# Kernel tuning notes

Hardware: AMD Instinct MI355X
Metric: run time of the kernel (lower is better)

## Reference

```python
import jax, jax.numpy as jnp
import numpy as np

WIN = 8          # window side -> N = 64 tokens per window
HEADS = 8
NCAV = 2
EGO_DIST_BINS = 4
EGO_ANGLE_BINS = 4


def _rel_pos_index(wh, ww):
    # Swin-style relative position index, (wh*ww, wh*ww) int
    coords = np.stack(np.meshgrid(np.arange(wh), np.arange(ww), indexing='ij'))  # (2,wh,ww)
    flat = coords.reshape(2, -1)
    rel = (flat[:, :, None] - flat[:, None, :]).transpose(1, 2, 0).astype(np.int64)
    rel[:, :, 0] += wh - 1
    rel[:, :, 1] += ww - 1
    rel[:, :, 0] *= 2 * ww - 1
    return jnp.asarray(rel.sum(-1))


def _ego_bias_index(affine_matrix, H, W):
    # per-(cav,window) bin index into ego_position_bias_table
    gy, gx = jnp.meshgrid(jnp.arange(H // WIN), jnp.arange(W // WIN), indexing='ij')
    centers = jnp.stack([gx * WIN + WIN / 2.0, gy * WIN + WIN / 2.0], axis=-1)
    centers = centers.reshape(-1, 2).astype(jnp.float32)              # (nW, 2)
    img_c = jnp.array([[W / 2.0], [H / 2.0]], jnp.float32)            # (2, 1)
    ego = (affine_matrix[:, :2, :2] @ img_c + affine_matrix[:, :2, 2:3])[..., 0]  # (ncav, 2)
    rel = centers[None, :, :] - ego[:, None, :]                        # (ncav, nW, 2)
    dist = jnp.linalg.norm(rel, axis=-1)
    ang = jnp.arctan2(rel[..., 1], rel[..., 0])
    db = (dist / (dist.max() + 1e-6) * (EGO_DIST_BINS - 1)).astype(jnp.int32)
    ab = ((ang + jnp.pi) / (2 * jnp.pi) * (EGO_ANGLE_BINS - 1)).astype(jnp.int32)
    return (db * EGO_ANGLE_BINS + ab).reshape(-1)                      # (ncav*nW,) == (B_,)


def setup_inputs() -> dict:
    key = jax.random.key(0)
    ks = jax.random.split(key, 10)
    H = W = 256
    B_ = NCAV * (H // WIN) * (W // WIN)   # 2048
    N = WIN * WIN                          # 64
    C = 256
    s = 0.02
    return {
        'x': jax.random.normal(ks[0], (B_, N, C), jnp.float32),
        'affine_matrix': jax.random.normal(ks[1], (NCAV, 2, 3), jnp.float32),
        'Wq': jax.random.normal(ks[2], (C, C), jnp.float32) * s,
        'bq': jax.random.normal(ks[3], (C,), jnp.float32) * s,
        'Wkv': jax.random.normal(ks[4], (C, 2 * C), jnp.float32) * s,
        'bkv': jax.random.normal(ks[5], (2 * C,), jnp.float32) * s,
        'Wp': jax.random.normal(ks[6], (C, C), jnp.float32) * s,
        'bp': jax.random.normal(ks[7], (C,), jnp.float32) * s,
        'rel_table': jax.random.normal(ks[8], ((2 * WIN - 1) ** 2, HEADS), jnp.float32) * s,
        'ego_table': jax.random.normal(ks[9], (EGO_DIST_BINS * EGO_ANGLE_BINS, HEADS), jnp.float32) * s,
        'w': jnp.ones((2,), jnp.float32),
        'H': H,
        'W': W,
    }


def reference(x, affine_matrix, Wq, bq, Wkv, bkv, Wp, bp, rel_table, ego_table, w, H, W):
    B_, N, C = x.shape
    h = HEADS
    hd = C // h
    scale = hd ** -0.5

    q = (x @ Wq + bq).reshape(B_, N, h, hd).transpose(0, 2, 1, 3)          # (B_, h, N, hd)
    kv = (x @ Wkv + bkv).reshape(B_, N, 2, h, hd).transpose(2, 0, 3, 1, 4)
    k, v = kv[0], kv[1]                                                     # (B_, h, N, hd)

    attn = jnp.einsum('bhnd,bhmd->bhnm', q * scale, k)                      # (B_, h, N, N)

    # Swin relative position bias
    rpi = _rel_pos_index(WIN, WIN)
    rel_bias = rel_table[rpi.reshape(-1)].reshape(N, N, h).transpose(2, 0, 1)  # (h, N, N)

    # ego-relative bias: one scalar per (window, head), broadcast over NxN
    idx = _ego_bias_index(affine_matrix, H, W)                              # (B_,)
    ego_bias = ego_table[idx]                                               # (B_, h)

    attn = attn + rel_bias[None, :, :, :] + ego_bias[:, :, None, None]

    attn0 = jax.nn.softmax(attn, axis=-1)
    attn1 = jnp.square(jnp.maximum(attn, 0.0))   # relu(attn)**2 (no-mask branch)
    ws = jax.nn.softmax(w)
    attn = attn0 * ws[0] + attn1 * ws[1]

    out = jnp.einsum('bhnm,bhmd->bhnd', attn, v).transpose(0, 2, 1, 3).reshape(B_, N, C)
    return out @ Wp + bp
```

## Files before the change

### kernel.cpp

```cpp
#include <hip/hip_runtime.h>

#define NT   64
#define CDIM 256
#define NHEAD 8
#define SCALE 0.17677669529663687f
#define PI_F 3.14159265358979f

typedef short bfrag __attribute__((ext_vector_type(8)));
typedef float f4    __attribute__((ext_vector_type(4)));
typedef unsigned short us4 __attribute__((ext_vector_type(4)));

__device__ __forceinline__ unsigned short f2bf(float f){
  unsigned u = __builtin_bit_cast(unsigned, f);
  u += 0x7FFFu + ((u >> 16) & 1u);
  return (unsigned short)(u >> 16);
}
__device__ __forceinline__ unsigned pk2(float a, float b){
  return (unsigned)f2bf(a) | ((unsigned)f2bf(b) << 16);
}
__device__ __forceinline__ f4 mfma16(bfrag a, bfrag b, f4 c){
  return __builtin_amdgcn_mfma_f32_16x16x32_bf16(a, b, c, 0, 0, 0);
}
__device__ __forceinline__ int swx(int row, int u){ return (row << 5) + (u ^ (row & 7)); }

__device__ __forceinline__ bfrag xpose(f4 m0, f4 m1, int quad, int cc){
  int P0m0 = (int)pk2(m0[0], m0[1]);
  int P1m0 = (int)pk2(m0[2], m0[3]);
  int P0m1 = (int)pk2(m1[0], m1[1]);
  int P1m1 = (int)pk2(m1[2], m1[3]);
  int srcA = ((quad & 1) << 5) + cc;
  int srcB = srcA + 16;
  int hi = quad >> 1;
  int a0 = __shfl(P0m0, srcA, 64), a1 = __shfl(P0m1, srcA, 64);
  int b0 = __shfl(P1m0, srcA, 64), b1 = __shfl(P1m1, srcA, 64);
  int c0 = __shfl(P0m0, srcB, 64), c1 = __shfl(P0m1, srcB, 64);
  int d0 = __shfl(P1m0, srcB, 64), d1 = __shfl(P1m1, srcB, 64);
  union { bfrag f; int u[4]; } r;
  r.u[0] = hi ? a1 : a0;
  r.u[1] = hi ? b1 : b0;
  r.u[2] = hi ? c1 : c0;
  r.u[3] = hi ? d1 : d0;
  return r.f;
}

__device__ __forceinline__ void subgemm32(const unsigned short* __restrict__ wt,
                                          const unsigned short* lx,
                                          const float* __restrict__ bqkv,
                                          int ocb, int tb, int quad, int cc,
                                          bfrag& f0, bfrag& f1)
{
  f4 acc[2][2];
  acc[0][0] = (f4){0,0,0,0}; acc[0][1] = (f4){0,0,0,0};
  acc[1][0] = (f4){0,0,0,0}; acc[1][1] = (f4){0,0,0,0};
  #pragma unroll
  for (int ks = 0; ks < 8; ++ks){
    bfrag a0 = *(const bfrag*)(wt + (ocb +      cc)*256 + ks*32 + quad*8);
    bfrag a1 = *(const bfrag*)(wt + (ocb + 16 + cc)*256 + ks*32 + quad*8);
    bfrag b0 = *(const bfrag*)(&lx[swx(tb +      cc, ks*4 + quad)*8]);
    bfrag b1 = *(const bfrag*)(&lx[swx(tb + 16 + cc, ks*4 + quad)*8]);
    acc[0][0] = mfma16(a0, b0, acc[0][0]);
    acc[0][1] = mfma16(a0, b1, acc[0][1]);
    acc[1][0] = mfma16(a1, b0, acc[1][0]);
    acc[1][1] = mfma16(a1, b1, acc[1][1]);
  }
  #pragma unroll
  for (int mt = 0; mt < 2; ++mt)
    #pragma unroll
    for (int r = 0; r < 4; ++r){
      float bb = bqkv[ocb + mt*16 + quad*4 + r];
      acc[mt][0][r] += bb;
      acc[mt][1][r] += bb;
    }
  f0 = xpose(acc[0][0], acc[1][0], quad, cc);
  f1 = xpose(acc[0][1], acc[1][1], quad, cc);
}

__device__ __forceinline__ void logits_it(bfrag aq, const bfrag* kf,
    int iibase, int quad, int cc, int h,
    const float* __restrict__ relt, float ego,
    f4 (&SA)[4], float (&Z)[4])
{
  #pragma unroll
  for (int jt = 0; jt < 4; ++jt){
    f4 z = (f4){0,0,0,0};
    SA[jt] = mfma16(aq, kf[jt], z);
  }
  #pragma unroll
  for (int jt = 0; jt < 4; ++jt){
    int jj = jt*16 + cc;
    int yj = jj >> 3, xj = jj & 7;
    #pragma unroll
    for (int r = 0; r < 4; ++r){
      int ii = iibase + r;
      int ridx = ((ii >> 3) - yj + 7)*15 + ((ii & 7) - xj + 7);
      SA[jt][r] += relt[ridx*8 + h] + ego;
    }
  }
  #pragma unroll
  for (int r = 0; r < 4; ++r){
    float m = fmaxf(fmaxf(SA[0][r], SA[1][r]), fmaxf(SA[2][r], SA[3][r]));
    for (int off = 1; off < 16; off <<= 1) m = fmaxf(m, __shfl_xor(m, off, 64));
    float s = 0.0f;
    #pragma unroll
    for (int jt = 0; jt < 4; ++jt) s += __expf(SA[jt][r] - m);
    for (int off = 1; off < 16; off <<= 1) s += __shfl_xor(s, off, 64);
    Z[r] = m + __logf(s);
  }
}

__device__ __forceinline__ void pv_it(const f4 (&SA)[4], const float (&Z)[4],
    int quad, int cc, unsigned short* Pt, const unsigned short* vts,
    float ws0, float ws1, f4* yit)
{
  #pragma unroll
  for (int chunk = 0; chunk < 2; ++chunk){
    #pragma unroll
    for (int jtl = 0; jtl < 2; ++jtl){
      int jt = chunk*2 + jtl;
      #pragma unroll
      for (int r = 0; r < 4; ++r){
        float av = SA[jt][r];
        float rl = fmaxf(av, 0.0f);
        float p = ws0 * __expf(av - Z[r]) + ws1 * rl * rl;
        Pt[(quad*4 + r)*32 + jtl*16 + cc] = f2bf(p);
      }
    }
    bfrag pa = *(const bfrag*)(&Pt[cc*32 + quad*8]);
    #pragma unroll
    for (int nt = 0; nt < 2; ++nt){
      int row = nt*16 + cc;
      bfrag pb = *(const bfrag*)(&vts[row*64 + (((chunk*4 + quad) ^ (row & 7)) << 3)]);
      yit[nt] = mfma16(pa, pb, yit[nt]);
    }
  }
}

__global__ void prep_kernel(const float* __restrict__ Wq,  const float* __restrict__ bq,
                            const float* __restrict__ Wkv, const float* __restrict__ bkv,
                            const float* __restrict__ Wp,
                            unsigned short* __restrict__ wt, float* __restrict__ bqkv)
{
  const int bid = blockIdx.x, tid = threadIdx.x;
  if (bid < 256) {
    __shared__ float t[32][33];
    const int r0 = (bid >> 3) * 32;
    const int c0 = (bid & 7) * 32;
    const int rl = tid & 31, ch = tid >> 5;
    for (int k = 0; k < 4; ++k){
      int c = c0 + ch + k*8, r = r0 + rl;
      float v;
      if (r < 256)      v = Wq[c*256 + r] * SCALE;
      else if (r < 768) v = Wkv[c*512 + (r - 256)];
      else              v = Wp[c*256 + (r - 768)];
      t[rl][ch + k*8] = v;
    }
    __syncthreads();
    for (int k = 0; k < 4; ++k){
      int orr = ch + k*8;
      wt[(r0 + orr)*256 + c0 + rl] = f2bf(t[orr][rl]);
    }
  } else {
    for (int j = tid; j < 768; j += 256)
      bqkv[j] = (j < 256) ? bq[j]*SCALE : bkv[j - 256];
  }
}

__global__ __launch_bounds__(512, 4) void attn_kernel(
    const float* __restrict__ x, const float* __restrict__ wvec,
    const float* __restrict__ bp, float* __restrict__ out,
    const unsigned short* __restrict__ wt, const float* __restrict__ bqkv,
    const float* __restrict__ relt, const float* __restrict__ egot,
    const float* __restrict__ aff)
{
  __shared__ unsigned short ldsX[NT*CDIM];
  __shared__ unsigned short ldsV[NHEAD*2048];
  __shared__ unsigned short ldsP[NHEAD*512];

  const int b = blockIdx.x;
  const int tid = threadIdx.x;
  const int wv = tid >> 6, lane = tid & 63;
  const int quad = lane >> 4, cc = lane & 15;
  const int h = wv;

  const float4* xg = (const float4*)(x + (size_t)b*(NT*CDIM));
  #pragma unroll
  for (int it = 0; it < 8; ++it){
    int i4 = tid + it*512;
    float4 v = xg[i4];
    us4 pk = { f2bf(v.x), f2bf(v.y), f2bf(v.z), f2bf(v.w) };
    int row = i4 >> 6, u = (i4 & 63) >> 1, hf = i4 & 1;
    *(us4*)(&ldsX[swx(row, u)*8 + hf*4]) = pk;
  }
  float w0 = wvec[0], w1 = wvec[1];
  float wm = fmaxf(w0, w1);
  float e0 = __expf(w0 - wm), e1 = __expf(w1 - wm);
  float ws0 = e0/(e0+e1), ws1 = e1/(e0+e1);
  float ego;
  {
    float ex0=(aff[0]+aff[1])*128.f+aff[2],  ey0=(aff[3]+aff[4])*128.f+aff[5];
    float ex1=(aff[6]+aff[7])*128.f+aff[8],  ey1=(aff[9]+aff[10])*128.f+aff[11];
    float dmax = 0.f;
    #pragma unroll
    for (int c = 0; c < 4; ++c){
      float cx = (c & 1) ? 252.f : 4.f, cy = (c >> 1) ? 252.f : 4.f;
      float d0x=cx-ex0, d0y=cy-ey0, d1x=cx-ex1, d1y=cy-ey1;
      dmax = fmaxf(dmax, fmaxf(sqrtf(d0x*d0x+d0y*d0y), sqrtf(d1x*d1x+d1y*d1y)));
    }
    dmax += 1e-6f;
    int cv = b >> 10, wi = b & 1023;
    float cx = (float)((wi & 31)*8 + 4), cy = (float)((wi >> 5)*8 + 4);
    float ex = cv ? ex1 : ex0, ey = cv ? ey1 : ey0;
    float dx = cx - ex, dy = cy - ey;
    float dd = sqrtf(dx*dx + dy*dy);
    float ang = atan2f(dy, dx);
    int db = (int)(dd/dmax*3.0f);
    int ab = (int)((ang + PI_F)/(2.0f*PI_F)*3.0f);
    ego = egot[(db*4 + ab)*8 + h];
  }
  __syncthreads();

  bfrag aq[4], kf[4];
  subgemm32(wt, ldsX, bqkv, h*32,       0,  quad, cc, aq[0], aq[1]);
  subgemm32(wt, ldsX, bqkv, h*32,       32, quad, cc, aq[2], aq[3]);
  subgemm32(wt, ldsX, bqkv, 256 + h*32, 0,  quad, cc, kf[0], kf[1]);
  subgemm32(wt, ldsX, bqkv, 256 + h*32, 32, quad, cc, kf[2], kf[3]);
  unsigned short* vs = &ldsV[wv*2048];
  {
    const int ocb = 512 + h*32;
    #pragma unroll
    for (int tb = 0; tb < 64; tb += 32){
      f4 vacc[2][2];
      vacc[0][0] = (f4){0,0,0,0}; vacc[0][1] = (f4){0,0,0,0};
      vacc[1][0] = (f4){0,0,0,0}; vacc[1][1] = (f4){0,0,0,0};
      #pragma unroll
      for (int ks = 0; ks < 8; ++ks){
        bfrag a0 = *(const bfrag*)(wt + (ocb +      cc)*256 + ks*32 + quad*8);
        bfrag a1 = *(const bfrag*)(wt + (ocb + 16 + cc)*256 + ks*32 + quad*8);
        bfrag b0 = *(const bfrag*)(&ldsX[swx(tb +      cc, ks*4 + quad)*8]);
        bfrag b1 = *(const bfrag*)(&ldsX[swx(tb + 16 + cc, ks*4 + quad)*8]);
        vacc[0][0] = mfma16(a0, b0, vacc[0][0]);
        vacc[0][1] = mfma16(a0, b1, vacc[0][1]);
        vacc[1][0] = mfma16(a1, b0, vacc[1][0]);
        vacc[1][1] = mfma16(a1, b1, vacc[1][1]);
      }
      #pragma unroll
      for (int mt = 0; mt < 2; ++mt)
        #pragma unroll
        for (int ntl = 0; ntl < 2; ++ntl){
          int tok = tb + ntl*16 + cc;
          int tu = tok >> 3, te = tok & 7;
          #pragma unroll
          for (int r = 0; r < 4; ++r){
            int d = mt*16 + quad*4 + r;
            vs[d*64 + ((tu ^ (d & 7)) << 3) + te] =
                f2bf(vacc[mt][ntl][r] + bqkv[ocb + d]);
          }
        }
    }
  }

  f4 yacc[4][2];
  #pragma unroll
  for (int it = 0; it < 4; ++it){
    yacc[it][0] = (f4){0,0,0,0}; yacc[it][1] = (f4){0,0,0,0};
  }
  unsigned short* Pt = &ldsP[wv*512];
  #pragma unroll
  for (int it = 0; it < 4; ++it){
    f4 SA[4]; float Z[4];
    logits_it(aq[it], kf, it*16 + quad*4, quad, cc, h, relt, ego, SA, Z);
    pv_it(SA, Z, quad, cc, Pt, vs, ws0, ws1, yacc[it]);
  }
  __syncthreads();

  #pragma unroll
  for (int it = 0; it < 4; ++it)
    #pragma unroll
    for (int nt = 0; nt < 2; ++nt)
      #pragma unroll
      for (int r = 0; r < 4; ++r){
        int ii = it*16 + quad*4 + r;
        int col = h*32 + nt*16 + cc;
        ldsX[swx(ii, col>>3)*8 + (col&7)] = f2bf(yacc[it][nt][r]);
      }
  __syncthreads();

  {
    const int mt = wv & 3;
    const int cb = (wv >> 2)*128;
    f4 o[8];
    #pragma unroll
    for (int nt = 0; nt < 8; ++nt) o[nt] = (f4){0,0,0,0};
    #pragma unroll
    for (int ks = 0; ks < 8; ++ks){
      bfrag ay = *(const bfrag*)(&ldsX[swx(mt*16 + cc, ks*4 + quad)*8]);
      #pragma unroll
      for (int nt = 0; nt < 8; ++nt){
        bfrag bw = *(const bfrag*)(wt + (768 + cb + nt*16 + cc)*256 + ks*32 + quad*8);
        o[nt] = mfma16(ay, bw, o[nt]);
      }
    }
    float* og = out + (size_t)b*(NT*CDIM);
    #pragma unroll
    for (int nt = 0; nt < 8; ++nt){
      int col = cb + nt*16 + cc;
      float bpv = bp[col];
      #pragma unroll
      for (int r = 0; r < 4; ++r){
        int tok = mt*16 + quad*4 + r;
        og[tok*256 + col] = o[nt][r] + bpv;
      }
    }
  }
}

extern "C" void kernel_launch(void* const* d_in, const int* in_sizes, int n_in,
                              void* d_out, int out_size, void* d_ws, size_t ws_size,
                              hipStream_t stream)
{
  const float* x    = (const float*)d_in[0];
  const float* aff  = (const float*)d_in[1];
  const float* Wq   = (const float*)d_in[2];
  const float* bq   = (const float*)d_in[3];
  const float* Wkv  = (const float*)d_in[4];
  const float* bkv  = (const float*)d_in[5];
  const float* Wp   = (const float*)d_in[6];
  const float* bp   = (const float*)d_in[7];
  const float* relt = (const float*)d_in[8];
  const float* egot = (const float*)d_in[9];
  const float* w    = (const float*)d_in[10];
  float* out = (float*)d_out;

  char* ws = (char*)d_ws;
  unsigned short* wt = (unsigned short*)ws;
  float* bqkv = (float*)(ws + 524288);

  hipLaunchKernelGGL(prep_kernel, dim3(257), dim3(256), 0, stream,
                     Wq, bq, Wkv, bkv, Wp, wt, bqkv);
  hipLaunchKernelGGL(attn_kernel, dim3(2048), dim3(512), 0, stream,
                     x, w, bp, out, wt, bqkv, relt, egot, aff);
}
```

Before: 570.5 us.

## Keep V and P in registers via transposed MFMA, drop LDS staging buffers

The V projection is computed in the transposed orientation and kept as register fragments via lane shuffles, so the per-head V and P staging buffers in shared memory are no longer needed. Logits are computed as K·Q^T so each lane holds a full query column, which turns the softmax reductions into two cross-quad shuffles. The probabilities are turned into MFMA operands with shuffles rather than an LDS round trip, and the attention output is written to LDS in MFMA-fragment order so the output projection reads it directly. This cuts LDS traffic and footprint, which may allow more blocks per CU, at the cost of more shuffles and register pressure.

```diff
diff --git a/kernel.cpp b/kernel.cpp
--- a/kernel.cpp
+++ b/kernel.cpp
@@ -49,90 +49,28 @@
                                           int ocb, int tb, int quad, int cc,
                                           bfrag& f0, bfrag& f1)
 {
-  f4 acc[2][2];
-  acc[0][0] = (f4){0,0,0,0}; acc[0][1] = (f4){0,0,0,0};
-  acc[1][0] = (f4){0,0,0,0}; acc[1][1] = (f4){0,0,0,0};
+  f4 acc00 = (f4){0,0,0,0}, acc01 = (f4){0,0,0,0};
+  f4 acc10 = (f4){0,0,0,0}, acc11 = (f4){0,0,0,0};
   #pragma unroll
   for (int ks = 0; ks < 8; ++ks){
     bfrag a0 = *(const bfrag*)(wt + (ocb +      cc)*256 + ks*32 + quad*8);
     bfrag a1 = *(const bfrag*)(wt + (ocb + 16 + cc)*256 + ks*32 + quad*8);
     bfrag b0 = *(const bfrag*)(&lx[swx(tb +      cc, ks*4 + quad)*8]);
     bfrag b1 = *(const bfrag*)(&lx[swx(tb + 16 + cc, ks*4 + quad)*8]);
-    acc[0][0] = mfma16(a0, b0, acc[0][0]);
-    acc[0][1] = mfma16(a0, b1, acc[0][1]);
-    acc[1][0] = mfma16(a1, b0, acc[1][0]);
-    acc[1][1] = mfma16(a1, b1, acc[1][1]);
-  }
-  #pragma unroll
-  for (int mt = 0; mt < 2; ++mt)
-    #pragma unroll
-    for (int r = 0; r < 4; ++r){
-      float bb = bqkv[ocb + mt*16 + quad*4 + r];
-      acc[mt][0][r] += bb;
-      acc[mt][1][r] += bb;
-    }
-  f0 = xpose(acc[0][0], acc[1][0], quad, cc);
-  f1 = xpose(acc[0][1], acc[1][1], quad, cc);
-}
-
-__device__ __forceinline__ void logits_it(bfrag aq, const bfrag* kf,
-    int iibase, int quad, int cc, int h,
-    const float* __restrict__ relt, float ego,
-    f4 (&SA)[4], float (&Z)[4])
-{
-  #pragma unroll
-  for (int jt = 0; jt < 4; ++jt){
-    f4 z = (f4){0,0,0,0};
-    SA[jt] = mfma16(aq, kf[jt], z);
-  }
-  #pragma unroll
-  for (int jt = 0; jt < 4; ++jt){
-    int jj = jt*16 + cc;
-    int yj = jj >> 3, xj = jj & 7;
-    #pragma unroll
-    for (int r = 0; r < 4; ++r){
-      int ii = iibase + r;
-      int ridx = ((ii >> 3) - yj + 7)*15 + ((ii & 7) - xj + 7);
-      SA[jt][r] += relt[ridx*8 + h] + ego;
-    }
+    acc00 = mfma16(a0, b0, acc00);
+    acc01 = mfma16(a0, b1, acc01);
+    acc10 = mfma16(a1, b0, acc10);
+    acc11 = mfma16(a1, b1, acc11);
   }
   #pragma unroll
   for (int r = 0; r < 4; ++r){
-    float m = fmaxf(fmaxf(SA[0][r], SA[1][r]), fmaxf(SA[2][r], SA[3][r]));
-    for (int off = 1; off < 16; off <<= 1) m = fmaxf(m, __shfl_xor(m, off, 64));
-    float s = 0.0f;
-    #pragma unroll
-    for (int jt = 0; jt < 4; ++jt) s += __expf(SA[jt][r] - m);
-    for (int off = 1; off < 16; off <<= 1) s += __shfl_xor(s, off, 64);
-    Z[r] = m + __logf(s);
-  }
-}
-
-__device__ __forceinline__ void pv_it(const f4 (&SA)[4], const float (&Z)[4],
-    int quad, int cc, unsigned short* Pt, const unsigned short* vts,
-    float ws0, float ws1, f4* yit)
-{
-  #pragma unroll
-  for (int chunk = 0; chunk < 2; ++chunk){
-    #pragma unroll
-    for (int jtl = 0; jtl < 2; ++jtl){
-      int jt = chunk*2 + jtl;
-      #pragma unroll
-      for (int r = 0; r < 4; ++r){
-        float av = SA[jt][r];
-        float rl = fmaxf(av, 0.0f);
-        float p = ws0 * __expf(av - Z[r]) + ws1 * rl * rl;
-        Pt[(quad*4 + r)*32 + jtl*16 + cc] = f2bf(p);
-      }
-    }
-    bfrag pa = *(const bfrag*)(&Pt[cc*32 + quad*8]);
-    #pragma unroll
-    for (int nt = 0; nt < 2; ++nt){
-      int row = nt*16 + cc;
-      bfrag pb = *(const bfrag*)(&vts[row*64 + (((chunk*4 + quad) ^ (row & 7)) << 3)]);
-      yit[nt] = mfma16(pa, pb, yit[nt]);
-    }
-  }
+    float bb0 = bqkv[ocb +      quad*4 + r];
+    float bb1 = bqkv[ocb + 16 + quad*4 + r];
+    acc00[r] += bb0; acc01[r] += bb0;
+    acc10[r] += bb1; acc11[r] += bb1;
+  }
+  f0 = xpose(acc00, acc10, quad, cc);
+  f1 = xpose(acc01, acc11, quad, cc);
 }
 
 __global__ void prep_kernel(const float* __restrict__ Wq,  const float* __restrict__ bq,
@@ -173,8 +111,6 @@
     const float* __restrict__ aff)
 {
   __shared__ unsigned short ldsX[NT*CDIM];
-  __shared__ unsigned short ldsV[NHEAD*2048];
-  __shared__ unsigned short ldsP[NHEAD*512];
 
   const int b = blockIdx.x;
   const int tid = threadIdx.x;
@@ -219,70 +155,85 @@
   }
   __syncthreads();
 
-  bfrag aq[4], kf[4];
-  subgemm32(wt, ldsX, bqkv, h*32,       0,  quad, cc, aq[0], aq[1]);
-  subgemm32(wt, ldsX, bqkv, h*32,       32, quad, cc, aq[2], aq[3]);
+  bfrag qf[4], kf[4], vf[4];
+  subgemm32(wt, ldsX, bqkv, h*32,       0,  quad, cc, qf[0], qf[1]);
+  subgemm32(wt, ldsX, bqkv, h*32,       32, quad, cc, qf[2], qf[3]);
   subgemm32(wt, ldsX, bqkv, 256 + h*32, 0,  quad, cc, kf[0], kf[1]);
   subgemm32(wt, ldsX, bqkv, 256 + h*32, 32, quad, cc, kf[2], kf[3]);
-  unsigned short* vs = &ldsV[wv*2048];
-  {
-    const int ocb = 512 + h*32;
-    #pragma unroll
-    for (int tb = 0; tb < 64; tb += 32){
-      f4 vacc[2][2];
-      vacc[0][0] = (f4){0,0,0,0}; vacc[0][1] = (f4){0,0,0,0};
-      vacc[1][0] = (f4){0,0,0,0}; vacc[1][1] = (f4){0,0,0,0};
-      #pragma unroll
-      for (int ks = 0; ks < 8; ++ks){
-        bfrag a0 = *(const bfrag*)(wt + (ocb +      cc)*256 + ks*32 + quad*8);
-        bfrag a1 = *(const bfrag*)(wt + (ocb + 16 + cc)*256 + ks*32 + quad*8);
-        bfrag b0 = *(const bfrag*)(&ldsX[swx(tb +      cc, ks*4 + quad)*8]);
-        bfrag b1 = *(const bfrag*)(&ldsX[swx(tb + 16 + cc, ks*4 + quad)*8]);
-        vacc[0][0] = mfma16(a0, b0, vacc[0][0]);
-        vacc[0][1] = mfma16(a0, b1, vacc[0][1]);
-        vacc[1][0] = mfma16(a1, b0, vacc[1][0]);
-        vacc[1][1] = mfma16(a1, b1, vacc[1][1]);
-      }
-      #pragma unroll
-      for (int mt = 0; mt < 2; ++mt)
-        #pragma unroll
-        for (int ntl = 0; ntl < 2; ++ntl){
-          int tok = tb + ntl*16 + cc;
-          int tu = tok >> 3, te = tok & 7;
-          #pragma unroll
-          for (int r = 0; r < 4; ++r){
-            int d = mt*16 + quad*4 + r;
-            vs[d*64 + ((tu ^ (d & 7)) << 3) + te] =
-                f2bf(vacc[mt][ntl][r] + bqkv[ocb + d]);
-          }
-        }
-    }
-  }
-
-  f4 yacc[4][2];
-  #pragma unroll
-  for (int it = 0; it < 4; ++it){
-    yacc[it][0] = (f4){0,0,0,0}; yacc[it][1] = (f4){0,0,0,0};
-  }
-  unsigned short* Pt = &ldsP[wv*512];
-  #pragma unroll
-  for (int it = 0; it < 4; ++it){
-    f4 SA[4]; float Z[4];
-    logits_it(aq[it], kf, it*16 + quad*4, quad, cc, h, relt, ego, SA, Z);
-    pv_it(SA, Z, quad, cc, Pt, vs, ws0, ws1, yacc[it]);
+  #pragma unroll
+  for (int chunk = 0; chunk < 2; ++chunk){
+    int tb = chunk*32;
+    f4 acc00 = (f4){0,0,0,0}, acc01 = (f4){0,0,0,0};
+    f4 acc10 = (f4){0,0,0,0}, acc11 = (f4){0,0,0,0};
+    #pragma unroll
+    for (int ks = 0; ks < 8; ++ks){
+      bfrag x0 = *(const bfrag*)(&ldsX[swx(tb +      cc, ks*4 + quad)*8]);
+      bfrag x1 = *(const bfrag*)(&ldsX[swx(tb + 16 + cc, ks*4 + quad)*8]);
+      bfrag w0f = *(const bfrag*)(wt + (512 + h*32 +      cc)*256 + ks*32 + quad*8);
+      bfrag w1f = *(const bfrag*)(wt + (512 + h*32 + 16 + cc)*256 + ks*32 + quad*8);
+      acc00 = mfma16(x0, w0f, acc00);
+      acc01 = mfma16(x0, w1f, acc01);
+      acc10 = mfma16(x1, w0f, acc10);
+      acc11 = mfma16(x1, w1f, acc11);
+    }
+    float bb0 = bqkv[512 + h*32 +      cc];
+    float bb1 = bqkv[512 + h*32 + 16 + cc];
+    #pragma unroll
+    for (int r = 0; r < 4; ++r){
+      acc00[r] += bb0; acc10[r] += bb0;
+      acc01[r] += bb1; acc11[r] += bb1;
+    }
+    vf[chunk*2 + 0] = xpose(acc00, acc10, quad, cc);
+    vf[chunk*2 + 1] = xpose(acc01, acc11, quad, cc);
   }
   __syncthreads();
 
-  #pragma unroll
-  for (int it = 0; it < 4; ++it)
-    #pragma unroll
-    for (int nt = 0; nt < 2; ++nt)
+  const f4 z4 = (f4){0,0,0,0};
+  #pragma unroll
+  for (int qt = 0; qt < 4; ++qt){
+    f4 SA[4];
+    #pragma unroll
+    for (int kt = 0; kt < 4; ++kt) SA[kt] = mfma16(kf[kt], qf[qt], z4);
+    int ii = qt*16 + cc;
+    int yi = ii >> 3, xi = ii & 7;
+    #pragma unroll
+    for (int kt = 0; kt < 4; ++kt)
       #pragma unroll
       for (int r = 0; r < 4; ++r){
-        int ii = it*16 + quad*4 + r;
-        int col = h*32 + nt*16 + cc;
-        ldsX[swx(ii, col>>3)*8 + (col&7)] = f2bf(yacc[it][nt][r]);
-      }
+        int jj = kt*16 + quad*4 + r;
+        int ridx = (yi - (jj >> 3) + 7)*15 + (xi - (jj & 7) + 7);
+        SA[kt][r] += relt[ridx*8 + h] + ego;
+      }
+    float m = -1e30f;
+    #pragma unroll
+    for (int kt = 0; kt < 4; ++kt)
+      #pragma unroll
+      for (int r = 0; r < 4; ++r) m = fmaxf(m, SA[kt][r]);
+    m = fmaxf(m, __shfl_xor(m, 16, 64));
+    m = fmaxf(m, __shfl_xor(m, 32, 64));
+    float s = 0.0f;
+    #pragma unroll
+    for (int kt = 0; kt < 4; ++kt)
+      #pragma unroll
+      for (int r = 0; r < 4; ++r) s += __expf(SA[kt][r] - m);
+    s += __shfl_xor(s, 16, 64);
+    s += __shfl_xor(s, 32, 64);
+    float Z = m + __logf(s);
+    #pragma unroll
+    for (int kt = 0; kt < 4; ++kt)
+      #pragma unroll
+      for (int r = 0; r < 4; ++r){
+        float av = SA[kt][r];
+        float rl = fmaxf(av, 0.0f);
+        SA[kt][r] = ws0 * __expf(av - Z) + ws1 * rl * rl;
+      }
+    bfrag p0 = xpose(SA[0], SA[1], quad, cc);
+    bfrag p1 = xpose(SA[2], SA[3], quad, cc);
+    f4 yT0 = mfma16(vf[0], p0, z4); yT0 = mfma16(vf[2], p1, yT0);
+    f4 yT1 = mfma16(vf[1], p0, z4); yT1 = mfma16(vf[3], p1, yT1);
+    bfrag yf = xpose(yT0, yT1, quad, cc);
+    *(bfrag*)(&ldsX[((qt*8 + h)*64 + lane)*8]) = yf;
+  }
   __syncthreads();
 
   {
@@ -293,7 +244,7 @@
     for (int nt = 0; nt < 8; ++nt) o[nt] = (f4){0,0,0,0};
     #pragma unroll
     for (int ks = 0; ks < 8; ++ks){
-      bfrag ay = *(const bfrag*)(&ldsX[swx(mt*16 + cc, ks*4 + quad)*8]);
+      bfrag ay = *(const bfrag*)(&ldsX[((mt*8 + ks)*64 + lane)*8]);
       #pragma unroll
       for (int nt = 0; nt < 8; ++nt){
         bfrag bw = *(const bfrag*)(wt + (768 + cb + nt*16 + cc)*256 + ks*32 + quad*8);
```

After: 661.4 us. 15.9% more time.
